# Kernel tuning notes

Measured on AMD Instinct MI355X. Metric: run time of the kernel, lower is better.

The kernel has to match this reference:

```python
import jax, jax.numpy as jnp
import numpy as np

ROPE_BASE = 1000000.0
EPS = 1e-6
N_HEADS = 16

def apply_rope(x, base=ROPE_BASE):
    # x: [b, seq, heads, head_dim]
    b, seq, n_heads, dim = x.shape
    half = dim // 2
    i = jnp.arange(half)
    theta = 1.0 / base ** (2 * i / dim)
    pos = jnp.arange(seq)
    angles = pos[:, None] * theta[None, :]            # [seq, half]
    cos = jnp.cos(angles)[None, :, None, :]
    sin = jnp.sin(angles)[None, :, None, :]
    x1, x2 = jnp.split(x, 2, axis=-1)
    return jnp.concatenate([x1 * cos - x2 * sin, x1 * sin + x2 * cos], axis=-1)

def setup_inputs() -> dict:
    key = jax.random.key(0)
    ks = jax.random.split(key, 6)
    b, seq, dim = 2, 2048, 1024
    scale = 1.0 / np.sqrt(dim)
    return {
        "x": jax.random.normal(ks[0], (b, seq, dim), dtype=jnp.float32),
        "norm_scale": jnp.ones((dim,), dtype=jnp.float32),
        "Wq": jax.random.normal(ks[1], (dim, dim), dtype=jnp.float32) * scale,
        "Wk": jax.random.normal(ks[2], (dim, dim), dtype=jnp.float32) * scale,
        "Wv": jax.random.normal(ks[3], (dim, dim), dtype=jnp.float32) * scale,
        "Wo": jax.random.normal(ks[4], (dim, dim), dtype=jnp.float32) * scale,
    }

def reference(x, norm_scale, Wq, Wk, Wv, Wo):
    b, seq, d = x.shape
    n_heads = N_HEADS
    dh = d // n_heads
    # RMSNorm
    var = jnp.mean(jnp.square(x), axis=-1, keepdims=True)
    x_norm = x * jax.lax.rsqrt(var + EPS) * norm_scale
    # QKV projections ([in,out] weights as in nnx.Linear)
    q = (x_norm @ Wq).reshape(b, seq, n_heads, dh)
    k = (x_norm @ Wk).reshape(b, seq, n_heads, dh)
    v = (x_norm @ Wv).reshape(b, seq, n_heads, dh)
    q = apply_rope(q)
    k = apply_rope(k)
    # causal attention with explicit score matrix (faithful to source)
    scores = jnp.einsum('bthd,bshd->bhts', q, k) / jnp.sqrt(jnp.float32(dh))
    causal = jnp.triu(jnp.full((seq, seq), -jnp.inf, dtype=jnp.float32), k=1)
    scores = scores + causal[None, None, :, :]
    weights = jax.nn.softmax(scores, axis=-1)
    out = jnp.einsum('bhts,bshd->bthd', weights, v).reshape(b, seq, d)
    return out @ Wo
```

## Files before the change

### kernel.cpp

```cpp
#include <hip/hip_runtime.h>

typedef unsigned short ushort_t;
typedef __attribute__((ext_vector_type(8))) short short8;
typedef __attribute__((ext_vector_type(4))) short short4v;
typedef __attribute__((ext_vector_type(4))) float floatx4;

#define DEV static __device__ __forceinline__
#define NEG_BIG (-1e30f)

typedef const __attribute__((address_space(1))) unsigned int* gas_ptr;
typedef __attribute__((address_space(3))) unsigned int* las_ptr;

DEV void async16(const ushort_t* g, ushort_t* l) {
    __builtin_amdgcn_global_load_lds((gas_ptr)(const void*)g, (las_ptr)(void*)l, 16, 0, 0);
}

DEV float bf2f(ushort_t u) {
    union { unsigned u; float f; } v; v.u = ((unsigned)u) << 16; return v.f;
}
DEV ushort_t f2bf(float f) {
    union { float f; unsigned u; } v; v.f = f;
    unsigned r = v.u + 0x7FFF + ((v.u >> 16) & 1);
    return (ushort_t)(r >> 16);
}
DEV ushort_t f2bf_trunc(float f) {
    union { float f; unsigned u; } v; v.f = f;
    return (ushort_t)(v.u >> 16);
}
DEV float load_bf16_scrub(const ushort_t* p, size_t i) {
    ushort_t u = p[i];
    if (((u >> 7) & 0xFF) == 0xFF) u = 0;
    return bf2f(u);
}
DEV float load_f32_scrub(const ushort_t* p, size_t i) {
    unsigned u = ((const unsigned*)p)[i];
    if (((u >> 23) & 0xFF) == 0xFF) u = 0;
    union { unsigned u; float f; } v; v.u = u; return v.f;
}

DEV int probe_is_f32(const ushort_t* __restrict__ p) {
    int tid = threadIdx.x + threadIdx.y * blockDim.x;
    int nthr = blockDim.x * blockDim.y;
    __shared__ int cnt;
    if (tid == 0) cnt = 0;
    __syncthreads();
    int weird = 0;
    for (int i = tid; i < 2048; i += nthr) {
        unsigned e = (p[i] >> 7) & 0xFF;
        weird += (e >= 0x90) ? 1 : 0;
    }
#pragma unroll
    for (int off = 32; off; off >>= 1) weird += __shfl_xor(weird, off);
    if ((tid & 63) == 0) atomicAdd(&cnt, weird);
    __syncthreads();
    return cnt > 16;
}

__global__ void prep_kernel(const ushort_t* __restrict__ W0,
                            const ushort_t* __restrict__ W1,
                            const ushort_t* __restrict__ W2,
                            const ushort_t* __restrict__ W3,
                            ushort_t* __restrict__ WTq3,
                            ushort_t* __restrict__ WoT,
                            const ushort_t* __restrict__ x,
                            const ushort_t* __restrict__ g,
                            ushort_t* __restrict__ xn) {
    int is_f32 = probe_is_f32(x);
    int z = blockIdx.z;
    if (z < 4) {
        const ushort_t* W = (z == 0) ? W0 : (z == 1) ? W1 : (z == 2) ? W2 : W3;
        __shared__ ushort_t tile[32][33];
        int tx = threadIdx.x, ty = threadIdx.y;
        int xx = blockIdx.x * 32 + tx;
        int y0 = blockIdx.y * 32;
#pragma unroll
        for (int j = 0; j < 32; j += 8) {
            size_t idx = (size_t)(y0 + ty + j) * 1024 + xx;
            tile[ty + j][tx] = f2bf(is_f32 ? load_f32_scrub(W, idx) : load_bf16_scrub(W, idx));
        }
        __syncthreads();
        int nx = blockIdx.y * 32 + tx;
        ushort_t* dst = (z < 3) ? WTq3 : WoT;
        int ny0 = blockIdx.x * 32 + ((z < 3) ? z * 1024 : 0);
#pragma unroll
        for (int j = 0; j < 32; j += 8)
            dst[(size_t)(ny0 + ty + j) * 1024 + nx] = tile[tx][ty + j];
    } else {
        int row = (z - 4) * 1024 + blockIdx.y * 32 + blockIdx.x;
        int tid = threadIdx.y * 32 + threadIdx.x;
        float vals[4], gv[4];
        size_t base = (size_t)row * 1024 + tid * 4;
#pragma unroll
        for (int i = 0; i < 4; i++) {
            if (is_f32) {
                vals[i] = load_f32_scrub(x, base + i);
                gv[i]   = load_f32_scrub(g, tid * 4 + i);
            } else {
                vals[i] = load_bf16_scrub(x, base + i);
                gv[i]   = load_bf16_scrub(g, tid * 4 + i);
            }
        }
        float ss = vals[0]*vals[0] + vals[1]*vals[1] + vals[2]*vals[2] + vals[3]*vals[3];
#pragma unroll
        for (int off = 32; off > 0; off >>= 1) ss += __shfl_xor(ss, off);
        __shared__ float red[4];
        if ((tid & 63) == 0) red[tid >> 6] = ss;
        __syncthreads();
        ss = red[0] + red[1] + red[2] + red[3];
        float inv = rsqrtf(ss * (1.0f / 1024.0f) + 1e-6f);
#pragma unroll
        for (int i = 0; i < 4; i++)
            xn[base + i] = f2bf(vals[i] * inv * gv[i]);
    }
}

__global__ __launch_bounds__(256, 4) void gemm_qkv(const ushort_t* __restrict__ A,
                                                   const ushort_t* __restrict__ Bt,
                                                   ushort_t* __restrict__ qb,
                                                   ushort_t* __restrict__ kb,
                                                   ushort_t* __restrict__ vt) {
    const int K = 1024;
    int tid = threadIdx.x;
    int lane = tid & 63, w = tid >> 6;
    int c = lane & 15, quad = lane >> 4;
    int mh = w >> 1, nh = w & 1;
    int lin = blockIdx.y * gridDim.x + blockIdx.x;
    int xcd = lin & 7, idx = lin >> 3;
    int bm = ((xcd & 3) * 8 + (idx & 7)) * 128;
    int bn = ((xcd >> 2) * 12 + (idx >> 3)) * 128;
    int lr = lane >> 2, lq = lane & 3;

    __shared__ __align__(16) ushort_t As[16 * 512];
    __shared__ __align__(16) ushort_t Bs[16 * 512];

    const floatx4 zero = {0.f, 0.f, 0.f, 0.f};
    floatx4 acc[4][4];
#pragma unroll
    for (int i = 0; i < 4; i++)
#pragma unroll
        for (int j = 0; j < 4; j++) acc[i][j] = zero;

    for (int k0 = 0; k0 < K; k0 += 64) {
        __syncthreads();
#pragma unroll
        for (int ci = 0; ci < 8; ci++) {
            int ch = w * 8 + ci;
            if (ch < 16) {
                int rg = ch >> 1, kc = ch & 1;
                async16(A + (size_t)(bm + rg * 16 + lr) * K + k0 + kc * 32 + lq * 8,
                        As + ch * 512);
            } else {
                int b2 = ch - 16;
                int rg = b2 >> 1, kc = b2 & 1;
                async16(Bt + (size_t)(bn + rg * 16 + lr) * K + k0 + kc * 32 + lq * 8,
                        Bs + b2 * 512);
            }
        }
        __syncthreads();
#pragma unroll
        for (int kc = 0; kc < 2; kc++) {
            short8 af[4], bf[4];
#pragma unroll
            for (int i = 0; i < 4; i++)
                af[i] = *(const short8*)(As + ((mh * 4 + i) * 2 + kc) * 512 + c * 32 + quad * 8);
#pragma unroll
            for (int j = 0; j < 4; j++)
                bf[j] = *(const short8*)(Bs + ((nh * 4 + j) * 2 + kc) * 512 + c * 32 + quad * 8);
#pragma unroll
            for (int i = 0; i < 4; i++)
#pragma unroll
                for (int j = 0; j < 4; j++)
                    acc[i][j] = __builtin_amdgcn_mfma_f32_16x16x32_bf16(af[i], bf[j], acc[i][j], 0, 0, 0);
        }
    }

    int proj = bn >> 10;
    int n0 = (bn & 1023) + nh * 64;
    if (proj < 2) {
        float th0 = exp2f((float)c * (-19.931568569324174f / 32.0f));
        float th1 = exp2f((float)(16 + c) * (-19.931568569324174f / 32.0f));
        float scale = (proj == 0) ? 0.125f : 1.0f;
#pragma unroll
        for (int i = 0; i < 4; i++)
#pragma unroll
            for (int r = 0; r < 4; r++) {
                int s = (bm + mh * 64 + i * 16 + quad * 4 + r) & 2047;
                float a0 = (float)s * th0, a1 = (float)s * th1;
                float sn0 = __sinf(a0), cs0 = __cosf(a0);
                float sn1 = __sinf(a1), cs1 = __cosf(a1);
                float x1a = acc[i][0][r], x2a = acc[i][2][r];
                acc[i][0][r] = (x1a * cs0 - x2a * sn0) * scale;
                acc[i][2][r] = (x1a * sn0 + x2a * cs0) * scale;
                float x1b = acc[i][1][r], x2b = acc[i][3][r];
                acc[i][1][r] = (x1b * cs1 - x2b * sn1) * scale;
                acc[i][3][r] = (x1b * sn1 + x2b * cs1) * scale;
            }
        ushort_t* dst = (proj == 0) ? qb : kb;
#pragma unroll
        for (int i = 0; i < 4; i++)
#pragma unroll
            for (int j = 0; j < 4; j++)
#pragma unroll
                for (int r = 0; r < 4; r++) {
                    int row = bm + mh * 64 + i * 16 + quad * 4 + r;
                    dst[(size_t)row * 1024 + n0 + j * 16 + c] = f2bf(acc[i][j][r]);
                }
    } else {
#pragma unroll
        for (int i = 0; i < 4; i++) {
            int row0 = bm + mh * 64 + i * 16 + quad * 4;
            int b = row0 >> 11, s0v = row0 & 2047;
#pragma unroll
            for (int j = 0; j < 4; j++) {
                int col = n0 + j * 16 + c;
                int hh = col >> 6, dh = col & 63;
                short4v pk;
#pragma unroll
                for (int r = 0; r < 4; r++) pk[r] = (short)f2bf(acc[i][j][r]);
                *(short4v*)(vt + (size_t)((b * 16 + hh) * 64 + dh) * 2048 + s0v) = pk;
            }
        }
    }
}

__global__ __launch_bounds__(256, 4) void gemm_out(const ushort_t* __restrict__ A,
                                                   const ushort_t* __restrict__ Bt,
                                                   float* __restrict__ C) {
    const int K = 1024, N = 1024;
    int tid = threadIdx.x;
    int lane = tid & 63, w = tid >> 6;
    int c = lane & 15, quad = lane >> 4;
    int mh = w >> 1, nh = w & 1;
    int lin = blockIdx.y * gridDim.x + blockIdx.x;
    int xcd = lin & 7, idx = lin >> 3;
    int bm = ((xcd & 3) * 8 + (idx & 7)) * 128;
    int bn = ((xcd >> 2) * 8 + (idx >> 3)) * 64;
    int lr = lane >> 2, lq = lane & 3;

    __shared__ __align__(16) ushort_t As[16 * 512];
    __shared__ __align__(16) ushort_t Bs[8 * 512];

    const floatx4 zero = {0.f, 0.f, 0.f, 0.f};
    floatx4 acc[4][2];
#pragma unroll
    for (int i = 0; i < 4; i++)
#pragma unroll
        for (int j = 0; j < 2; j++) acc[i][j] = zero;

    for (int k0 = 0; k0 < K; k0 += 64) {
        __syncthreads();
#pragma unroll
        for (int ci = 0; ci < 6; ci++) {
            int ch = w * 6 + ci;
            if (ch < 16) {
                int rg = ch >> 1, kc = ch & 1;
                async16(A + (size_t)(bm + rg * 16 + lr) * K + k0 + kc * 32 + lq * 8,
                        As + ch * 512);
            } else {
                int b2 = ch - 16;
                int rg = b2 >> 1, kc = b2 & 1;
                async16(Bt + (size_t)(bn + rg * 16 + lr) * K + k0 + kc * 32 + lq * 8,
                        Bs + b2 * 512);
            }
        }
        __syncthreads();
#pragma unroll
        for (int kc = 0; kc < 2; kc++) {
            short8 af[4], bf[2];
#pragma unroll
            for (int i = 0; i < 4; i++)
                af[i] = *(const short8*)(As + ((mh * 4 + i) * 2 + kc) * 512 + c * 32 + quad * 8);
#pragma unroll
            for (int j = 0; j < 2; j++)
                bf[j] = *(const short8*)(Bs + ((nh * 2 + j) * 2 + kc) * 512 + c * 32 + quad * 8);
#pragma unroll
            for (int i = 0; i < 4; i++)
#pragma unroll
                for (int j = 0; j < 2; j++)
                    acc[i][j] = __builtin_amdgcn_mfma_f32_16x16x32_bf16(af[i], bf[j], acc[i][j], 0, 0, 0);
        }
    }
#pragma unroll
    for (int i = 0; i < 4; i++)
#pragma unroll
        for (int j = 0; j < 2; j++)
#pragma unroll
            for (int r = 0; r < 4; r++) {
                int row = bm + mh * 64 + i * 16 + quad * 4 + r;
                int col = bn + nh * 32 + j * 16 + c;
                C[(size_t)row * N + col] = acc[i][j][r];
            }
}

__global__ __launch_bounds__(256) void attn_kernel(const ushort_t* __restrict__ q,
                                                   const ushort_t* __restrict__ k,
                                                   const ushort_t* __restrict__ vt,
                                                   ushort_t* __restrict__ o) {
    int tid = threadIdx.x;
    int lane = tid & 63, w = tid >> 6;
    int c = lane & 15, quad = lane >> 4;
    int bh = blockIdx.x;
    int b = bh >> 4, h = bh & 15;
    int qt = 31 - (int)blockIdx.y;
    int lr = lane >> 2, lq = lane & 3;
    const ushort_t* qb  = q + (size_t)b * 2048 * 1024 + h * 64;
    const ushort_t* kbp = k + (size_t)b * 2048 * 1024 + h * 64;
    const ushort_t* vtb = vt + (size_t)(b * 16 + h) * 64 * 2048;
    ushort_t* ob = o + (size_t)b * 2048 * 1024 + h * 64;

    __shared__ __align__(16) ushort_t Ks[2][8 * 512];
    __shared__ __align__(16) ushort_t Vs[2][8 * 512];
    __shared__ __align__(16) ushort_t Ps[64 * 64];

    const floatx4 zero = {0.f, 0.f, 0.f, 0.f};

    int t0b = qt * 64;
    int t0w = t0b + w * 16;
    int ntile = qt + 1;

    const ushort_t* qrow = qb + (size_t)(t0w + c) * 1024;
    short8 aq0 = *(const short8*)(qrow + quad * 8);
    short8 aq1 = *(const short8*)(qrow + 32 + quad * 8);

    int pswz = (c & 7) << 3;
    int pwbase = ((w * 16 + c) * 64) ;
    int prbase = ((w * 16 + c) * 64) ;

    float l_sum = 0.f;
    floatx4 oacc[4];
#pragma unroll
    for (int dt = 0; dt < 4; dt++) oacc[dt] = zero;

#pragma unroll
    for (int ci = 0; ci < 4; ci++) {
        int ch = w * 4 + ci;
        if (ch < 8) {
            int nt = ch >> 1, hf = ch & 1;
            async16(kbp + (size_t)(nt * 16 + lr) * 1024 + hf * 32 + lq * 8,
                    Ks[0] + ch * 512);
        } else {
            int dt = (ch - 8) >> 1, hf = ch & 1;
            async16(vtb + (size_t)(dt * 16 + lr) * 2048 + hf * 32 + lq * 8,
                    Vs[0] + (ch - 8) * 512);
        }
    }

    for (int kt = 0; kt < ntile; kt++) {
        __syncthreads();
        int cur = kt & 1;
        if (kt + 1 < ntile) {
            int s1 = (kt + 1) * 64;
            int nxt = cur ^ 1;
#pragma unroll
            for (int ci = 0; ci < 4; ci++) {
                int ch = w * 4 + ci;
                if (ch < 8) {
                    int nt = ch >> 1, hf = ch & 1;
                    async16(kbp + (size_t)(s1 + nt * 16 + lr) * 1024 + hf * 32 + lq * 8,
                            Ks[nxt] + ch * 512);
                } else {
                    int dt = (ch - 8) >> 1, hf = ch & 1;
                    async16(vtb + (size_t)(dt * 16 + lr) * 2048 + s1 + hf * 32 + lq * 8,
                            Vs[nxt] + (ch - 8) * 512);
                }
            }
        }
        int s0 = kt * 64;

        floatx4 sacc[4];
#pragma unroll
        for (int nt = 0; nt < 4; nt++) sacc[nt] = zero;
#pragma unroll
        for (int nt = 0; nt < 4; nt++) {
            short8 k0f = *(const short8*)(Ks[cur] + nt * 1024 + c * 32 + quad * 8);
            short8 k1f = *(const short8*)(Ks[cur] + nt * 1024 + 512 + c * 32 + quad * 8);
            sacc[nt] = __builtin_amdgcn_mfma_f32_16x16x32_bf16(k0f, aq0, sacc[nt], 0, 0, 0);
            sacc[nt] = __builtin_amdgcn_mfma_f32_16x16x32_bf16(k1f, aq1, sacc[nt], 0, 0, 0);
        }

        if (kt == ntile - 1) {
            int t = t0w + c;
#pragma unroll
            for (int nt = 0; nt < 4; nt++) {
                short4v pk;
                float pn = 0.f;
#pragma unroll
                for (int r = 0; r < 4; r++) {
                    int s = s0 + nt * 16 + quad * 4 + r;
                    float e = __expf((s > t) ? NEG_BIG : sacc[nt][r]);
                    pn += e;
                    pk[r] = (short)f2bf_trunc(e);
                }
                l_sum += pn;
                *(short4v*)(Ps + ((pwbase + nt * 16 + quad * 4) ^ pswz)) = pk;
            }
        } else {
#pragma unroll
            for (int nt = 0; nt < 4; nt++) {
                short4v pk;
                float pn = 0.f;
#pragma unroll
                for (int r = 0; r < 4; r++) {
                    float e = __expf(sacc[nt][r]);
                    pn += e;
                    pk[r] = (short)f2bf_trunc(e);
                }
                l_sum += pn;
                *(short4v*)(Ps + ((pwbase + nt * 16 + quad * 4) ^ pswz)) = pk;
            }
        }

        short8 pa0 = *(const short8*)(Ps + ((prbase + quad * 8) ^ pswz));
        short8 pa1 = *(const short8*)(Ps + ((prbase + 32 + quad * 8) ^ pswz));
#pragma unroll
        for (int dt = 0; dt < 4; dt++) {
            short8 v0 = *(const short8*)(Vs[cur] + dt * 1024 + c * 32 + quad * 8);
            short8 v1 = *(const short8*)(Vs[cur] + dt * 1024 + 512 + c * 32 + quad * 8);
            oacc[dt] = __builtin_amdgcn_mfma_f32_16x16x32_bf16(pa0, v0, oacc[dt], 0, 0, 0);
            oacc[dt] = __builtin_amdgcn_mfma_f32_16x16x32_bf16(pa1, v1, oacc[dt], 0, 0, 0);
        }
    }

    float l = l_sum;
    l += __shfl_xor(l, 16);
    l += __shfl_xor(l, 32);
    float linv0 = 1.0f / l;
    float linv[4];
#pragma unroll
    for (int r = 0; r < 4; r++) linv[r] = __shfl(linv0, quad * 4 + r);

#pragma unroll
    for (int dt = 0; dt < 4; dt++)
#pragma unroll
        for (int r = 0; r < 4; r++) {
            int t = t0w + quad * 4 + r;
            ob[(size_t)t * 1024 + dt * 16 + c] = f2bf_trunc(oacc[dt][r] * linv[r]);
        }
}

extern "C" void kernel_launch(void* const* d_in, const int* in_sizes, int n_in,
                              void* d_out, int out_size, void* d_ws, size_t ws_size,
                              hipStream_t stream) {
    const ushort_t* x  = (const ushort_t*)d_in[0];
    const ushort_t* g  = (const ushort_t*)d_in[1];
    const ushort_t* Wq = (const ushort_t*)d_in[2];
    const ushort_t* Wk = (const ushort_t*)d_in[3];
    const ushort_t* Wv = (const ushort_t*)d_in[4];
    const ushort_t* Wo = (const ushort_t*)d_in[5];

    char* ws = (char*)d_ws;
    const size_t MB = 1ull << 20;
    ushort_t* xn   = (ushort_t*)(ws);
    ushort_t* qb   = (ushort_t*)(ws + 8 * MB);
    ushort_t* kb   = (ushort_t*)(ws + 16 * MB);
    ushort_t* vt   = (ushort_t*)(ws + 24 * MB);
    ushort_t* WTq3 = (ushort_t*)(ws + 32 * MB);
    ushort_t* WoT  = (ushort_t*)(ws + 38 * MB);
    ushort_t* at   = xn;

    prep_kernel<<<dim3(32, 32, 8), dim3(32, 8), 0, stream>>>(Wq, Wk, Wv, Wo, WTq3, WoT, x, g, xn);

    gemm_qkv<<<dim3(24, 32), 256, 0, stream>>>(xn, WTq3, qb, kb, vt);

    attn_kernel<<<dim3(32, 32), 256, 0, stream>>>(qb, kb, vt, at);

    gemm_out<<<dim3(16, 32), 256, 0, stream>>>(at, WoT, (float*)d_out);
}
```

Measured before the change: 183.3 us.

## Enlarge attention query tile to 128 rows so each K/V tile is reused twice

The attention kernel now handles 128 query rows per block instead of 64, and each wave processes two 16-row groups. Every K/V tile loaded into shared memory therefore feeds twice as many MFMAs. This halves the total K/V global traffic and halves the grid size. Waves whose rows lie entirely before a tile skip it after the barrier. The cost is higher register pressure, a larger P buffer, fewer blocks (512), and more causal imbalance within a block.

```diff
diff --git a/kernel.cpp b/kernel.cpp
--- a/kernel.cpp
+++ b/kernel.cpp
@@ -301,7 +301,7 @@
     int c = lane & 15, quad = lane >> 4;
     int bh = blockIdx.x;
     int b = bh >> 4, h = bh & 15;
-    int qt = 31 - (int)blockIdx.y;
+    int qt = 15 - (int)blockIdx.y;
     int lr = lane >> 2, lq = lane & 3;
     const ushort_t* qb  = q + (size_t)b * 2048 * 1024 + h * 64;
     const ushort_t* kbp = k + (size_t)b * 2048 * 1024 + h * 64;
@@ -310,26 +310,30 @@
 
     __shared__ __align__(16) ushort_t Ks[2][8 * 512];
     __shared__ __align__(16) ushort_t Vs[2][8 * 512];
-    __shared__ __align__(16) ushort_t Ps[64 * 64];
+    __shared__ __align__(16) ushort_t Ps[128 * 64];
 
     const floatx4 zero = {0.f, 0.f, 0.f, 0.f};
 
-    int t0b = qt * 64;
-    int t0w = t0b + w * 16;
-    int ntile = qt + 1;
-
-    const ushort_t* qrow = qb + (size_t)(t0w + c) * 1024;
-    short8 aq0 = *(const short8*)(qrow + quad * 8);
-    short8 aq1 = *(const short8*)(qrow + 32 + quad * 8);
+    int t0b = qt * 128;
+    int t0w = t0b + w * 32;
+    int ntile = 2 * (qt + 1);
+
+    const ushort_t* qr0 = qb + (size_t)(t0w + c) * 1024;
+    const ushort_t* qr1 = qb + (size_t)(t0w + 16 + c) * 1024;
+    short8 aq[2][2];
+    aq[0][0] = *(const short8*)(qr0 + quad * 8);
+    aq[0][1] = *(const short8*)(qr0 + 32 + quad * 8);
+    aq[1][0] = *(const short8*)(qr1 + quad * 8);
+    aq[1][1] = *(const short8*)(qr1 + 32 + quad * 8);
 
     int pswz = (c & 7) << 3;
-    int pwbase = ((w * 16 + c) * 64) ;
-    int prbase = ((w * 16 + c) * 64) ;
-
-    float l_sum = 0.f;
-    floatx4 oacc[4];
-#pragma unroll
-    for (int dt = 0; dt < 4; dt++) oacc[dt] = zero;
+
+    float l_sum[2] = {0.f, 0.f};
+    floatx4 oacc[2][4];
+#pragma unroll
+    for (int g = 0; g < 2; g++)
+#pragma unroll
+        for (int dt = 0; dt < 4; dt++) oacc[g][dt] = zero;
 
 #pragma unroll
     for (int ci = 0; ci < 4; ci++) {
@@ -366,76 +370,100 @@
             }
         }
         int s0 = kt * 64;
-
-        floatx4 sacc[4];
-#pragma unroll
-        for (int nt = 0; nt < 4; nt++) sacc[nt] = zero;
+        if (s0 > t0w + 31) continue;
+
+        floatx4 sacc[2][4];
+#pragma unroll
+        for (int g = 0; g < 2; g++)
+#pragma unroll
+            for (int nt = 0; nt < 4; nt++) sacc[g][nt] = zero;
 #pragma unroll
         for (int nt = 0; nt < 4; nt++) {
             short8 k0f = *(const short8*)(Ks[cur] + nt * 1024 + c * 32 + quad * 8);
             short8 k1f = *(const short8*)(Ks[cur] + nt * 1024 + 512 + c * 32 + quad * 8);
-            sacc[nt] = __builtin_amdgcn_mfma_f32_16x16x32_bf16(k0f, aq0, sacc[nt], 0, 0, 0);
-            sacc[nt] = __builtin_amdgcn_mfma_f32_16x16x32_bf16(k1f, aq1, sacc[nt], 0, 0, 0);
-        }
-
-        if (kt == ntile - 1) {
-            int t = t0w + c;
-#pragma unroll
-            for (int nt = 0; nt < 4; nt++) {
-                short4v pk;
-                float pn = 0.f;
-#pragma unroll
-                for (int r = 0; r < 4; r++) {
-                    int s = s0 + nt * 16 + quad * 4 + r;
-                    float e = __expf((s > t) ? NEG_BIG : sacc[nt][r]);
-                    pn += e;
-                    pk[r] = (short)f2bf_trunc(e);
+#pragma unroll
+            for (int g = 0; g < 2; g++) {
+                sacc[g][nt] = __builtin_amdgcn_mfma_f32_16x16x32_bf16(k0f, aq[g][0], sacc[g][nt], 0, 0, 0);
+                sacc[g][nt] = __builtin_amdgcn_mfma_f32_16x16x32_bf16(k1f, aq[g][1], sacc[g][nt], 0, 0, 0);
+            }
+        }
+
+        if (s0 + 63 > t0w) {
+#pragma unroll
+            for (int g = 0; g < 2; g++) {
+                int t = t0w + g * 16 + c;
+                int pwbase = (w * 32 + g * 16 + c) * 64;
+#pragma unroll
+                for (int nt = 0; nt < 4; nt++) {
+                    short4v pk;
+                    float pn = 0.f;
+#pragma unroll
+                    for (int r = 0; r < 4; r++) {
+                        int s = s0 + nt * 16 + quad * 4 + r;
+                        float e = __expf((s > t) ? NEG_BIG : sacc[g][nt][r]);
+                        pn += e;
+                        pk[r] = (short)f2bf_trunc(e);
+                    }
+                    l_sum[g] += pn;
+                    *(short4v*)(Ps + ((pwbase + nt * 16 + quad * 4) ^ pswz)) = pk;
                 }
-                l_sum += pn;
-                *(short4v*)(Ps + ((pwbase + nt * 16 + quad * 4) ^ pswz)) = pk;
             }
         } else {
 #pragma unroll
-            for (int nt = 0; nt < 4; nt++) {
-                short4v pk;
-                float pn = 0.f;
-#pragma unroll
-                for (int r = 0; r < 4; r++) {
-                    float e = __expf(sacc[nt][r]);
-                    pn += e;
-                    pk[r] = (short)f2bf_trunc(e);
+            for (int g = 0; g < 2; g++) {
+                int pwbase = (w * 32 + g * 16 + c) * 64;
+#pragma unroll
+                for (int nt = 0; nt < 4; nt++) {
+                    short4v pk;
+                    float pn = 0.f;
+#pragma unroll
+                    for (int r = 0; r < 4; r++) {
+                        float e = __expf(sacc[g][nt][r]);
+                        pn += e;
+                        pk[r] = (short)f2bf_trunc(e);
+                    }
+                    l_sum[g] += pn;
+                    *(short4v*)(Ps + ((pwbase + nt * 16 + quad * 4) ^ pswz)) = pk;
                 }
-                l_sum += pn;
-                *(short4v*)(Ps + ((pwbase + nt * 16 + quad * 4) ^ pswz)) = pk;
-            }
-        }
-
-        short8 pa0 = *(const short8*)(Ps + ((prbase + quad * 8) ^ pswz));
-        short8 pa1 = *(const short8*)(Ps + ((prbase + 32 + quad * 8) ^ pswz));
+            }
+        }
+
+        short8 pa[2][2];
+#pragma unroll
+        for (int g = 0; g < 2; g++) {
+            int prbase = (w * 32 + g * 16 + c) * 64;
+            pa[g][0] = *(const short8*)(Ps + ((prbase + quad * 8) ^ pswz));
+            pa[g][1] = *(const short8*)(Ps + ((prbase + 32 + quad * 8) ^ pswz));
+        }
 #pragma unroll
         for (int dt = 0; dt < 4; dt++) {
             short8 v0 = *(const short8*)(Vs[cur] + dt * 1024 + c * 32 + quad * 8);
             short8 v1 = *(const short8*)(Vs[cur] + dt * 1024 + 512 + c * 32 + quad * 8);
-            oacc[dt] = __builtin_amdgcn_mfma_f32_16x16x32_bf16(pa0, v0, oacc[dt], 0, 0, 0);
-            oacc[dt] = __builtin_amdgcn_mfma_f32_16x16x32_bf16(pa1, v1, oacc[dt], 0, 0, 0);
-        }
-    }
-
-    float l = l_sum;
-    l += __shfl_xor(l, 16);
-    l += __shfl_xor(l, 32);
-    float linv0 = 1.0f / l;
-    float linv[4];
-#pragma unroll
-    for (int r = 0; r < 4; r++) linv[r] = __shfl(linv0, quad * 4 + r);
-
-#pragma unroll
-    for (int dt = 0; dt < 4; dt++)
-#pragma unroll
-        for (int r = 0; r < 4; r++) {
-            int t = t0w + quad * 4 + r;
-            ob[(size_t)t * 1024 + dt * 16 + c] = f2bf_trunc(oacc[dt][r] * linv[r]);
-        }
+#pragma unroll
+            for (int g = 0; g < 2; g++) {
+                oacc[g][dt] = __builtin_amdgcn_mfma_f32_16x16x32_bf16(pa[g][0], v0, oacc[g][dt], 0, 0, 0);
+                oacc[g][dt] = __builtin_amdgcn_mfma_f32_16x16x32_bf16(pa[g][1], v1, oacc[g][dt], 0, 0, 0);
+            }
+        }
+    }
+
+#pragma unroll
+    for (int g = 0; g < 2; g++) {
+        float l = l_sum[g];
+        l += __shfl_xor(l, 16);
+        l += __shfl_xor(l, 32);
+        float linv0 = 1.0f / l;
+        float linv[4];
+#pragma unroll
+        for (int r = 0; r < 4; r++) linv[r] = __shfl(linv0, quad * 4 + r);
+#pragma unroll
+        for (int dt = 0; dt < 4; dt++)
+#pragma unroll
+            for (int r = 0; r < 4; r++) {
+                int t = t0w + g * 16 + quad * 4 + r;
+                ob[(size_t)t * 1024 + dt * 16 + c] = f2bf_trunc(oacc[g][dt][r] * linv[r]);
+            }
+    }
 }
 
 extern "C" void kernel_launch(void* const* d_in, const int* in_sizes, int n_in,
@@ -462,7 +490,7 @@
 
     gemm_qkv<<<dim3(24, 32), 256, 0, stream>>>(xn, WTq3, qb, kb, vt);
 
-    attn_kernel<<<dim3(32, 32), 256, 0, stream>>>(qb, kb, vt, at);
+    attn_kernel<<<dim3(32, 16), 256, 0, stream>>>(qb, kb, vt, at);
 
     gemm_out<<<dim3(16, 32), 256, 0, stream>>>(at, WoT, (float*)d_out);
 }
```

Result: slower. 194.4 us (+6.1%).
